# Performance work log

Hardware: AMD Instinct MI355X
Metric: run time of the kernel (lower is better)

The kernel has to match this reference:

```python
import jax, jax.numpy as jnp
import numpy as np

D_MODEL = 1024
D_INTERNAL = 256


def setup_inputs() -> dict:
    key = jax.random.key(0)
    ks = jax.random.split(key, 12)
    s = 0.02
    return {
        "x": jax.random.normal(ks[0], (4, 2048, D_MODEL), dtype=jnp.float32),
        "Wq": jax.random.normal(ks[1], (D_MODEL, D_INTERNAL), dtype=jnp.float32) * s,
        "bq": jnp.zeros((D_INTERNAL,), dtype=jnp.float32),
        "Wk": jax.random.normal(ks[2], (D_MODEL, D_INTERNAL), dtype=jnp.float32) * s,
        "bk": jnp.zeros((D_INTERNAL,), dtype=jnp.float32),
        "Wv": jax.random.normal(ks[3], (D_MODEL, D_MODEL), dtype=jnp.float32) * s,
        "bv": jnp.zeros((D_MODEL,), dtype=jnp.float32),
        "W1": jax.random.normal(ks[4], (D_MODEL, D_MODEL), dtype=jnp.float32) * s,
        "b1": jnp.zeros((D_MODEL,), dtype=jnp.float32),
        "W2": jax.random.normal(ks[5], (D_MODEL, D_MODEL), dtype=jnp.float32) * s,
        "b2": jnp.zeros((D_MODEL,), dtype=jnp.float32),
    }


def reference(x, Wq, bq, Wk, bk, Wv, bv, W1, b1, W2, b2):
    # x: [B, S, D]
    S = x.shape[-2]
    q = x @ Wq + bq            # [B, S, Di]
    k = x @ Wk + bk            # [B, S, Di]
    v = x @ Wv + bv            # [B, S, D]
    scale = 1.0 / jnp.sqrt(jnp.asarray(q.shape[-1], dtype=x.dtype))
    scores = jnp.einsum('bqd,bkd->bqk', q, k) * scale  # [B, S, S]
    causal_mask = jnp.triu(jnp.ones((S, S), dtype=bool), k=1)
    scores = jnp.where(causal_mask, -jnp.inf, scores)
    attn = jax.nn.softmax(scores, axis=-1)             # [B, S, S]
    attention = jnp.einsum('bqk,bkd->bqd', attn, v)    # [B, S, D]
    h = x + attention
    ff = jax.nn.relu(h @ W1 + b1) @ W2 + b2
    return h + ff, attn
```

## Files before the change

### kernel.cpp

```cpp
#include <hip/hip_runtime.h>
#include <hip/hip_bf16.h>

#define BM 128
#define BN 128

typedef __bf16 bf16x8 __attribute__((ext_vector_type(8)));
typedef float f32x4 __attribute__((ext_vector_type(4)));
typedef unsigned short u16;

__device__ __forceinline__ u16 f2bf(float f) {
    __bf16 b = (__bf16)f;
    return __builtin_bit_cast(u16, b);
}
__device__ __forceinline__ float bf2f(u16 u) {
    __bf16 b = __builtin_bit_cast(__bf16, u);
    return (float)b;
}

__device__ __forceinline__ void gload_lds16(const void* g, void* l) {
    __builtin_amdgcn_global_load_lds(
        (const __attribute__((address_space(1))) void*)g,
        (__attribute__((address_space(3))) void*)l,
        16, 0, 0);
}

__device__ __forceinline__ bf16x8 lds_read_b128(const u16* p) {
    bf16x8 r;
    const __attribute__((address_space(3))) u16* lp =
        (const __attribute__((address_space(3))) u16*)p;
    asm volatile("ds_read_b128 %0, %1" : "=v"(r) : "v"(lp));
    return r;
}

template <int MODE>
__global__ __launch_bounds__(256)
void gemm_bt(const u16* __restrict__ A, int lda, long long a_bs,
             const u16* __restrict__ Bt, int ldb, long long b_bs,
             int Kdim, int ldc, long long c_bs,
             const float* __restrict__ bias, float scale,
             const void* __restrict__ resid, long long r_bs,
             void* __restrict__ out, int causal)
{
    int bx = blockIdx.x, by = blockIdx.y, bz = blockIdx.z;
    if (causal == 3) {
        const int t = blockIdx.x;
        int byy = (int)((sqrtf(8.f * (float)t + 1.f) - 1.f) * 0.5f);
        while ((byy + 1) * (byy + 2) / 2 <= t) byy++;
        while (byy * (byy + 1) / 2 > t) byy--;
        by = byy; bx = t - byy * (byy + 1) / 2; bz = blockIdx.y;
    }
    const int kend = Kdim;

    A  += (long long)bz * a_bs;
    Bt += (long long)bz * b_bs;

    const int m0 = by * BM, n0 = bx * BN;
    const int tid = threadIdx.x;
    const int wave = tid >> 6, lane = tid & 63;
    const int wy = wave >> 1, wx = wave & 1;
    const int lr = lane >> 2, lc8 = (lane & 3) * 8;
    const int lane15 = lane & 15, kq = lane >> 4;

    __shared__ __align__(16) u16 As[2][BM * 32];
    __shared__ __align__(16) u16 Bs[2][BN * 32];

    f32x4 acc[4][4] = {};

    for (int k0 = 0; k0 < kend; k0 += 64) {
        __syncthreads();
        #pragma unroll
        for (int h = 0; h < 2; h++) {
            const int kh = k0 + h * 32 + lc8;
            #pragma unroll
            for (int it = 0; it < 2; it++) {
                const int row = wave * 16 + it * 64 + lr;
                gload_lds16(A  + (size_t)(m0 + row) * lda + kh,
                            &As[h][(wave * 16 + it * 64) * 32]);
                gload_lds16(Bt + (size_t)(n0 + row) * ldb + kh,
                            &Bs[h][(wave * 16 + it * 64) * 32]);
            }
        }
        __syncthreads();

        #pragma unroll
        for (int h = 0; h < 2; h++) {
            bf16x8 av[4], bv[4];
            #pragma unroll
            for (int i = 0; i < 4; i++)
                av[i] = *(const bf16x8*)&As[h][(wy * 64 + i * 16 + lane15) * 32 + kq * 8];
            #pragma unroll
            for (int j = 0; j < 4; j++)
                bv[j] = *(const bf16x8*)&Bs[h][(wx * 64 + j * 16 + lane15) * 32 + kq * 8];
            #pragma unroll
            for (int i = 0; i < 4; i++)
                #pragma unroll
                for (int j = 0; j < 4; j++)
                    acc[i][j] = __builtin_amdgcn_mfma_f32_16x16x32_bf16(av[i], bv[j], acc[i][j], 0, 0, 0);
        }
    }

    #pragma unroll
    for (int i = 0; i < 4; i++) {
        const int rl = m0 + wy * 64 + i * 16 + kq * 4;
        #pragma unroll
        for (int j = 0; j < 4; j++) {
            const int c = n0 + wx * 64 + j * 16 + lane15;
            #pragma unroll
            for (int rg = 0; rg < 4; rg++) {
                const int r = rl + rg;
                const size_t idx = (size_t)bz * c_bs + (size_t)r * ldc + c;
                const float v = acc[i][j][rg];
                if (MODE == 2) {
                    float p = __expf(v * scale);
                    if (c > r) p = 0.f;
                    ((u16*)out)[idx] = f2bf(p);
                }
            }
        }
    }
}

template <int MODE>
__global__ __launch_bounds__(256, 2)
void gemm_bt3(const u16* __restrict__ A, int lda, long long a_bs,
              const u16* __restrict__ Bt, int ldb, long long b_bs,
              int Kdim, int ldc, long long c_bs,
              const float* __restrict__ bias,
              const void* __restrict__ resid, long long r_bs,
              void* __restrict__ out, int causal)
{
    int bx = blockIdx.x, by = blockIdx.y;
    const int bz = blockIdx.z;
    if (causal == 0) {
        const int gx = gridDim.x;
        const int nwg = gx * (int)gridDim.y;
        int lin = by * gx + bx;
        lin = (lin & 7) * (nwg >> 3) + (lin >> 3);
        by = lin / gx; bx = lin % gx;
    } else if (causal == 2 && bz >= 2) {
        by = (int)gridDim.y - 1 - by;
    }
    const int kend = (causal == 2) ? min(Kdim, (by + 1) * 128) : Kdim;
    const int NT = kend >> 6;

    A  += (long long)bz * a_bs;
    Bt += (long long)bz * b_bs;

    const int m0 = by * 128, n0 = bx * 128;
    const int tid = threadIdx.x;
    const int wave = tid >> 6, lane = tid & 63;
    const int wy = wave >> 1, wx = wave & 1;
    const int lane15 = lane & 15, kq = lane >> 4;
    const int lr = lane >> 2;
    const int swzc8 = ((lane & 3) ^ ((lane >> 3) & 3)) * 8;
    const int lslot = lane15 * 32 + ((kq ^ ((lane15 >> 1) & 3)) * 8);

    __shared__ __align__(16) u16 As[2][2][128 * 32];
    __shared__ __align__(16) u16 Bs[2][2][128 * 32];

    f32x4 acc[4][4] = {};

    auto stage = [&](int buf, int tt) {
        #pragma unroll
        for (int h = 0; h < 2; h++) {
            const int kh = (tt << 6) + h * 32 + swzc8;
            #pragma unroll
            for (int it = 0; it < 2; it++) {
                const int row = wave * 16 + it * 64 + lr;
                gload_lds16(A + (size_t)(m0 + row) * lda + kh,
                            &As[buf][h][(wave * 16 + it * 64) * 32]);
                gload_lds16(Bt + (size_t)(n0 + row) * ldb + kh,
                            &Bs[buf][h][(wave * 16 + it * 64) * 32]);
            }
        }
    };

    stage(0, 0);

    for (int t = 0; t < NT; t++) {
        const int cur = t & 1;
        if (t) __builtin_amdgcn_s_barrier();
        if (t + 1 < NT) {
            stage(cur ^ 1, t + 1);
            asm volatile("s_waitcnt vmcnt(8)" ::: "memory");
        } else {
            asm volatile("s_waitcnt vmcnt(0)" ::: "memory");
        }
        __builtin_amdgcn_s_barrier();

        bf16x8 av0[4], bv0[4], av1[4], bv1[4];
        #pragma unroll
        for (int i = 0; i < 4; i++)
            av0[i] = lds_read_b128(&As[cur][0][(wy * 64 + i * 16) * 32 + lslot]);
        #pragma unroll
        for (int j = 0; j < 4; j++)
            bv0[j] = lds_read_b128(&Bs[cur][0][(wx * 64 + j * 16) * 32 + lslot]);
        #pragma unroll
        for (int i = 0; i < 4; i++)
            av1[i] = lds_read_b128(&As[cur][1][(wy * 64 + i * 16) * 32 + lslot]);
        #pragma unroll
        for (int j = 0; j < 4; j++)
            bv1[j] = lds_read_b128(&Bs[cur][1][(wx * 64 + j * 16) * 32 + lslot]);

        asm volatile("s_waitcnt lgkmcnt(8)" ::: "memory");
        __builtin_amdgcn_sched_barrier(0);
        __builtin_amdgcn_s_setprio(1);
        #pragma unroll
        for (int i = 0; i < 4; i++)
            #pragma unroll
            for (int j = 0; j < 4; j++)
                acc[i][j] = __builtin_amdgcn_mfma_f32_16x16x32_bf16(av0[i], bv0[j], acc[i][j], 0, 0, 0);
        __builtin_amdgcn_s_setprio(0);

        asm volatile("s_waitcnt lgkmcnt(0)" ::: "memory");
        __builtin_amdgcn_sched_barrier(0);
        __builtin_amdgcn_s_setprio(1);
        #pragma unroll
        for (int i = 0; i < 4; i++)
            #pragma unroll
            for (int j = 0; j < 4; j++)
                acc[i][j] = __builtin_amdgcn_mfma_f32_16x16x32_bf16(av1[i], bv1[j], acc[i][j], 0, 0, 0);
        __builtin_amdgcn_s_setprio(0);
    }

    if (MODE == 6 && n0 >= 512) {
        u16* o = (u16*)resid;
        #pragma unroll
        for (int i = 0; i < 4; i++) {
            const int r = m0 + wy * 64 + i * 16 + kq * 4;
            const size_t base = (size_t)(r >> 11) * 1024 * 2048 + (r & 2047);
            #pragma unroll
            for (int j = 0; j < 4; j++) {
                const int c = n0 + wx * 64 + j * 16 + lane15;
                const float bj = bias[c];
                ushort4 pk;
                pk.x = f2bf(acc[i][j][0] + bj);
                pk.y = f2bf(acc[i][j][1] + bj);
                pk.z = f2bf(acc[i][j][2] + bj);
                pk.w = f2bf(acc[i][j][3] + bj);
                *(ushort4*)&o[base + (size_t)(c - 512) * 2048] = pk;
            }
        }
    } else {
        #pragma unroll
        for (int i = 0; i < 4; i++) {
            const int rl = m0 + wy * 64 + i * 16 + kq * 4;
            #pragma unroll
            for (int j = 0; j < 4; j++) {
                const int c = n0 + wx * 64 + j * 16 + lane15;
                float bj = 0.f;
                if (MODE == 4 || MODE == 5 || MODE == 6) bj = bias[c];
                #pragma unroll
                for (int rg = 0; rg < 4; rg++) {
                    const int r = rl + rg;
                    const size_t idx = (size_t)bz * c_bs + (size_t)r * ldc + c;
                    const float v = acc[i][j][rg];
                    if (MODE == 3) {
                        const u16* xr = (const u16*)resid;
                        const float linv = bias[(size_t)bz * 2048 + r];
                        const float h = bf2f(xr[(size_t)bz * r_bs + (size_t)r * ldc + c]) + v * linv;
                        ((u16*)out)[idx] = f2bf(h);
                    } else if (MODE == 4) {
                        ((u16*)out)[idx] = f2bf(fmaxf(v + bj, 0.f));
                    } else if (MODE == 5) {
                        const u16* hb = (const u16*)resid;
                        ((float*)out)[idx] = v + bj + bf2f(hb[(size_t)r * ldc + c]);
                    } else if (MODE == 6) {
                        ((u16*)out)[idx] = f2bf(v + bj);
                    }
                }
            }
        }
    }
}

__global__ __launch_bounds__(256)
void prep_x(const float* __restrict__ x, u16* __restrict__ xb)
{
    const int N4 = 8388608 / 4;
    for (int i = blockIdx.x * blockDim.x + threadIdx.x; i < N4; i += gridDim.x * blockDim.x) {
        const float4 v = ((const float4*)x)[i];
        ushort4 o;
        o.x = f2bf(v.x); o.y = f2bf(v.y); o.z = f2bf(v.z); o.w = f2bf(v.w);
        ((ushort4*)xb)[i] = o;
    }
}

__global__ __launch_bounds__(256)
void prep_w(const float* __restrict__ Wq, const float* __restrict__ bq,
            const float* __restrict__ Wk, const float* __restrict__ bk,
            const float* __restrict__ Wv, const float* __restrict__ bv,
            const float* __restrict__ b1, const float* __restrict__ b2,
            const float* __restrict__ W1, const float* __restrict__ W2,
            u16* __restrict__ WqkT, u16* __restrict__ WvT,
            u16* __restrict__ W1T, u16* __restrict__ W2T, float* __restrict__ biasv)
{
    const int bid = blockIdx.x, tid = threadIdx.x;
    if (bid == 896) {
        for (int t = tid; t < 3584; t += 256) {
            if (t < 512)       biasv[t] = (t < 256) ? bq[t] : bk[t - 256];
            else if (t < 1536) biasv[t] = bv[t - 512];
            else if (t < 2560) biasv[t] = b1[t - 1536];
            else               biasv[t] = b2[t - 2560];
        }
        return;
    }
    const float* src; u16* dst; int ld_src, kt, nt, nbase;
    if (bid < 128) {
        const int job = bid >> 6, t = bid & 63;
        src = job ? Wk : Wq; ld_src = 256;
        kt = t >> 2; nt = t & 3; nbase = job * 256 + nt * 64;
        dst = WqkT;
    } else {
        const int j = bid - 128, w = j >> 8, t = j & 255;
        src = (w == 0) ? Wv : (w == 1) ? W1 : W2; ld_src = 1024;
        kt = t >> 4; nt = t & 15; nbase = nt * 64;
        dst = (w == 0) ? WvT : (w == 1) ? W1T : W2T;
    }
    const int k0 = kt * 64;
    const int n0s = (ld_src == 256) ? (nbase & 255) : nbase;

    __shared__ float tile[64][65];
    const int ri = tid >> 4, j4 = (tid & 15) * 4;
    #pragma unroll
    for (int rr = 0; rr < 4; rr++) {
        const int i = ri + rr * 16;
        const float4 v = *(const float4*)&src[(size_t)(k0 + i) * ld_src + n0s + j4];
        tile[j4 + 0][i] = v.x;
        tile[j4 + 1][i] = v.y;
        tile[j4 + 2][i] = v.z;
        tile[j4 + 3][i] = v.w;
    }
    __syncthreads();
    const int n = tid >> 2, ks = (tid & 3) * 16;
    ushort4 o[4];
    #pragma unroll
    for (int c = 0; c < 4; c++) {
        o[c].x = f2bf(tile[n][ks + c * 4 + 0]);
        o[c].y = f2bf(tile[n][ks + c * 4 + 1]);
        o[c].z = f2bf(tile[n][ks + c * 4 + 2]);
        o[c].w = f2bf(tile[n][ks + c * 4 + 3]);
    }
    u16* drow = &dst[(size_t)(nbase + n) * 1024 + k0 + ks];
    #pragma unroll
    for (int c = 0; c < 4; c++) *(ushort4*)&drow[c * 4] = o[c];
}

__device__ __forceinline__ float wave_sum(float v) {
    #pragma unroll
    for (int off = 32; off > 0; off >>= 1) v += __shfl_xor(v, off, 64);
    return v;
}

__global__ __launch_bounds__(256)
void norm_kernel(const u16* __restrict__ attnb, float* __restrict__ attn,
                 float* __restrict__ linv)
{
    const int S = 2048;
    const int row = blockIdx.x;
    const int q = row & (S - 1);
    const int kpad = (q + 128) & ~127;
    const u16* brow = attnb + (size_t)row * S;
    float* srow = attn + (size_t)row * S;
    __shared__ float red[4];
    const int tid = threadIdx.x, wv = tid >> 6, ln = tid & 63;
    const int k = tid * 8;

    float vals[8];
    float lsum = 0.f;
    if (k < kpad) {
        const ushort4 a = *(const ushort4*)&brow[k];
        const ushort4 b = *(const ushort4*)&brow[k + 4];
        vals[0] = bf2f(a.x); vals[1] = bf2f(a.y); vals[2] = bf2f(a.z); vals[3] = bf2f(a.w);
        vals[4] = bf2f(b.x); vals[5] = bf2f(b.y); vals[6] = bf2f(b.z); vals[7] = bf2f(b.w);
        #pragma unroll
        for (int c = 0; c < 8; c++) lsum += vals[c];
    }
    lsum = wave_sum(lsum);
    if (ln == 0) red[wv] = lsum;
    __syncthreads();
    const float rinv = 1.f / (red[0] + red[1] + red[2] + red[3]);

    float4 o0 = {0.f, 0.f, 0.f, 0.f}, o1 = {0.f, 0.f, 0.f, 0.f};
    if (k < kpad) {
        o0 = make_float4(vals[0] * rinv, vals[1] * rinv, vals[2] * rinv, vals[3] * rinv);
        o1 = make_float4(vals[4] * rinv, vals[5] * rinv, vals[6] * rinv, vals[7] * rinv);
    }
    *(float4*)&srow[k] = o0;
    *(float4*)&srow[k + 4] = o1;
    if (tid == 0) linv[row] = rinv;
}

extern "C" void kernel_launch(void* const* d_in, const int* in_sizes, int n_in,
                              void* d_out, int out_size, void* d_ws, size_t ws_size,
                              hipStream_t stream)
{
    const float* x  = (const float*)d_in[0];
    const float* Wq = (const float*)d_in[1];
    const float* bq = (const float*)d_in[2];
    const float* Wk = (const float*)d_in[3];
    const float* bk = (const float*)d_in[4];
    const float* Wv = (const float*)d_in[5];
    const float* bv = (const float*)d_in[6];
    const float* W1 = (const float*)d_in[7];
    const float* b1 = (const float*)d_in[8];
    const float* W2 = (const float*)d_in[9];
    const float* b2 = (const float*)d_in[10];

    const int B = 4, S = 2048, D = 1024, BS = B * S;

    char* ws = (char*)d_ws;
    u16*   xb    = (u16*)(ws + 0);
    u16*   WqkT  = (u16*)(ws + 16777216);
    u16*   WvT   = (u16*)(ws + 17825792);
    u16*   W1T   = (u16*)(ws + 19922944);
    u16*   W2T   = (u16*)(ws + 22020096);
    float* biasv = (float*)(ws + 24117248);
    u16*   QK    = (u16*)(ws + 24133632);
    u16*   Vt    = (u16*)(ws + 32522240);
    u16*   attnb = (u16*)(ws + 49299456);
    float* linv  = (float*)(ws + 83886080);
    u16*   hb    = xb;
    u16*   ff1   = attnb;

    float* out0 = (float*)d_out;
    float* attn = out0 + (size_t)BS * D;

    const dim3 blk(256);

    prep_x<<<dim3(1024), blk, 0, stream>>>(x, xb);
    prep_w<<<dim3(897), blk, 0, stream>>>(Wq, bq, Wk, bk, Wv, bv, b1, b2, W1, W2,
                                          WqkT, WvT, W1T, W2T, biasv);

    gemm_bt3<6><<<dim3(12, 64, 1), blk, 0, stream>>>(
        xb, 1024, 0, WqkT, 1024, 0, 1024, 512, 0,
        biasv, Vt, 0, QK, 0);

    gemm_bt<2><<<dim3(136, 4, 1), blk, 0, stream>>>(
        QK, 512, (long long)S * 512, QK + 256, 512, (long long)S * 512,
        256, S, (long long)S * S, nullptr, 0.0625f, nullptr, 0, attnb, 3);

    norm_kernel<<<dim3(BS), blk, 0, stream>>>(attnb, attn, linv);

    gemm_bt3<3><<<dim3(8, 16, 4), blk, 0, stream>>>(
        attnb, S, (long long)S * S, Vt, S, (long long)D * S,
        S, D, (long long)S * D, linv, xb, (long long)S * D, hb, 2);

    gemm_bt3<4><<<dim3(8, 64, 1), blk, 0, stream>>>(
        hb, 1024, 0, W1T, 1024, 0, 1024, 1024, 0,
        biasv + 1536, nullptr, 0, ff1, 0);

    gemm_bt3<5><<<dim3(8, 64, 1), blk, 0, stream>>>(
        ff1, 1024, 0, W2T, 1024, 0, 1024, 1024, 0,
        biasv + 2560, hb, 0, out0, 0);
}
```

Measured before the change: 292.1 us.

## Deepen GEMM pipeline to four stages with BK=32 slots

```diff
diff --git a/kernel.cpp b/kernel.cpp
--- a/kernel.cpp
+++ b/kernel.cpp
@@ -122,7 +122,7 @@
 
 template <int MODE>
 __global__ __launch_bounds__(256, 2)
-void gemm_bt3(const u16* __restrict__ A, int lda, long long a_bs,
+void gemm_bt4(const u16* __restrict__ A, int lda, long long a_bs,
               const u16* __restrict__ Bt, int ldb, long long b_bs,
               int Kdim, int ldc, long long c_bs,
               const float* __restrict__ bias,
@@ -141,7 +141,7 @@
         by = (int)gridDim.y - 1 - by;
     }
     const int kend = (causal == 2) ? min(Kdim, (by + 1) * 128) : Kdim;
-    const int NT = kend >> 6;
+    const int NT = kend >> 5;
 
     A  += (long long)bz * a_bs;
     Bt += (long long)bz * b_bs;
@@ -155,72 +155,55 @@
     const int swzc8 = ((lane & 3) ^ ((lane >> 3) & 3)) * 8;
     const int lslot = lane15 * 32 + ((kq ^ ((lane15 >> 1) & 3)) * 8);
 
-    __shared__ __align__(16) u16 As[2][2][128 * 32];
-    __shared__ __align__(16) u16 Bs[2][2][128 * 32];
+    __shared__ __align__(16) u16 As[4][128 * 32];
+    __shared__ __align__(16) u16 Bs[4][128 * 32];
 
     f32x4 acc[4][4] = {};
 
-    auto stage = [&](int buf, int tt) {
-        #pragma unroll
-        for (int h = 0; h < 2; h++) {
-            const int kh = (tt << 6) + h * 32 + swzc8;
-            #pragma unroll
-            for (int it = 0; it < 2; it++) {
-                const int row = wave * 16 + it * 64 + lr;
-                gload_lds16(A + (size_t)(m0 + row) * lda + kh,
-                            &As[buf][h][(wave * 16 + it * 64) * 32]);
-                gload_lds16(Bt + (size_t)(n0 + row) * ldb + kh,
-                            &Bs[buf][h][(wave * 16 + it * 64) * 32]);
-            }
+    auto stage = [&](int slot, int tt) {
+        const int kh = (tt << 5) + swzc8;
+        #pragma unroll
+        for (int it = 0; it < 2; it++) {
+            const int row = wave * 16 + it * 64 + lr;
+            gload_lds16(A + (size_t)(m0 + row) * lda + kh,
+                        &As[slot][(wave * 16 + it * 64) * 32]);
+            gload_lds16(Bt + (size_t)(n0 + row) * ldb + kh,
+                        &Bs[slot][(wave * 16 + it * 64) * 32]);
         }
     };
 
-    stage(0, 0);
+    stage(0, 0); stage(1, 1); stage(2, 2);
 
     for (int t = 0; t < NT; t++) {
-        const int cur = t & 1;
+        const int cur = t & 3;
         if (t) __builtin_amdgcn_s_barrier();
-        if (t + 1 < NT) {
-            stage(cur ^ 1, t + 1);
+        if (t + 3 < NT) {
+            stage((t + 3) & 3, t + 3);
+            asm volatile("s_waitcnt vmcnt(12)" ::: "memory");
+        } else if (t == NT - 3) {
             asm volatile("s_waitcnt vmcnt(8)" ::: "memory");
+        } else if (t == NT - 2) {
+            asm volatile("s_waitcnt vmcnt(4)" ::: "memory");
         } else {
             asm volatile("s_waitcnt vmcnt(0)" ::: "memory");
         }
         __builtin_amdgcn_s_barrier();
 
-        bf16x8 av0[4], bv0[4], av1[4], bv1[4];
+        bf16x8 av[4], bv[4];
         #pragma unroll
         for (int i = 0; i < 4; i++)
-            av0[i] = lds_read_b128(&As[cur][0][(wy * 64 + i * 16) * 32 + lslot]);
+            av[i] = lds_read_b128(&As[cur][(wy * 64 + i * 16) * 32 + lslot]);
         #pragma unroll
         for (int j = 0; j < 4; j++)
-            bv0[j] = lds_read_b128(&Bs[cur][0][(wx * 64 + j * 16) * 32 + lslot]);
-        #pragma unroll
-        for (int i = 0; i < 4; i++)
-            av1[i] = lds_read_b128(&As[cur][1][(wy * 64 + i * 16) * 32 + lslot]);
-        #pragma unroll
-        for (int j = 0; j < 4; j++)
-            bv1[j] = lds_read_b128(&Bs[cur][1][(wx * 64 + j * 16) * 32 + lslot]);
-
-        asm volatile("s_waitcnt lgkmcnt(8)" ::: "memory");
-        __builtin_amdgcn_sched_barrier(0);
-        __builtin_amdgcn_s_setprio(1);
-        #pragma unroll
-        for (int i = 0; i < 4; i++)
-            #pragma unroll
-            for (int j = 0; j < 4; j++)
-                acc[i][j] = __builtin_amdgcn_mfma_f32_16x16x32_bf16(av0[i], bv0[j], acc[i][j], 0, 0, 0);
-        __builtin_amdgcn_s_setprio(0);
+            bv[j] = lds_read_b128(&Bs[cur][(wx * 64 + j * 16) * 32 + lslot]);
 
         asm volatile("s_waitcnt lgkmcnt(0)" ::: "memory");
         __builtin_amdgcn_sched_barrier(0);
-        __builtin_amdgcn_s_setprio(1);
         #pragma unroll
         for (int i = 0; i < 4; i++)
             #pragma unroll
             for (int j = 0; j < 4; j++)
-                acc[i][j] = __builtin_amdgcn_mfma_f32_16x16x32_bf16(av1[i], bv1[j], acc[i][j], 0, 0, 0);
-        __builtin_amdgcn_s_setprio(0);
+                acc[i][j] = __builtin_amdgcn_mfma_f32_16x16x32_bf16(av[i], bv[j], acc[i][j], 0, 0, 0);
     }
 
     if (MODE == 6 && n0 >= 512) {
@@ -432,7 +415,7 @@
     prep_w<<<dim3(897), blk, 0, stream>>>(Wq, bq, Wk, bk, Wv, bv, b1, b2, W1, W2,
                                           WqkT, WvT, W1T, W2T, biasv);
 
-    gemm_bt3<6><<<dim3(12, 64, 1), blk, 0, stream>>>(
+    gemm_bt4<6><<<dim3(12, 64, 1), blk, 0, stream>>>(
         xb, 1024, 0, WqkT, 1024, 0, 1024, 512, 0,
         biasv, Vt, 0, QK, 0);
 
@@ -442,15 +425,15 @@
 
     norm_kernel<<<dim3(BS), blk, 0, stream>>>(attnb, attn, linv);
 
-    gemm_bt3<3><<<dim3(8, 16, 4), blk, 0, stream>>>(
+    gemm_bt4<3><<<dim3(8, 16, 4), blk, 0, stream>>>(
         attnb, S, (long long)S * S, Vt, S, (long long)D * S,
         S, D, (long long)S * D, linv, xb, (long long)S * D, hb, 2);
 
-    gemm_bt3<4><<<dim3(8, 64, 1), blk, 0, stream>>>(
+    gemm_bt4<4><<<dim3(8, 64, 1), blk, 0, stream>>>(
         hb, 1024, 0, W1T, 1024, 0, 1024, 1024, 0,
         biasv + 1536, nullptr, 0, ff1, 0);
 
-    gemm_bt3<5><<<dim3(8, 64, 1), blk, 0, stream>>>(
+    gemm_bt4<5><<<dim3(8, 64, 1), blk, 0, stream>>>(
         ff1, 1024, 0, W2T, 1024, 0, 1024, 1024, 0,
         biasv + 2560, hb, 0, out0, 0);
 }
```

After: 298.5 us. 1.02x slower.
